# Performance work log

Measured on AMD Instinct MI355X. Metric: run time of the kernel, lower is better.

Reference implementation:

```python
import jax, jax.numpy as jnp
import numpy as np

B = 256
THRESH = 0.0
SHIFT = 0.0


def setup_inputs() -> dict:
    key = jax.random.key(0)
    ks = jax.random.split(key, 8)
    s = lambda k, shape, sc: (jax.random.normal(k, shape, jnp.float32) * sc)
    return {
        "x": jax.random.normal(ks[0], (B, 3, 250, 250), jnp.float32),
        "conv1_w": s(ks[1], (6, 3, 5, 5), 0.08),
        "conv1_b": jnp.zeros((6,), jnp.float32),
        "conv2_w": s(ks[2], (15, 6, 3, 3), 0.12),
        "conv2_b": jnp.zeros((15,), jnp.float32),
        "fc1_w": s(ks[3], (120, 55815), 0.004),
        "fc1_b": jnp.zeros((120,), jnp.float32),
        "fc2_w": s(ks[4], (84, 120), 0.09),
        "fc2_b": jnp.zeros((84,), jnp.float32),
        "fc3_w": s(ks[5], (1, 84), 0.1),
        "fc3_b": jnp.zeros((1,), jnp.float32),
        "pl_w": s(ks[6], (1, 1), 1.0),
        "pl_b": jnp.zeros((1,), jnp.float32),
        "pl_scale": jnp.ones((1,), jnp.float32),
        "pl_bias": jnp.zeros((1,), jnp.float32),
    }


def _conv2d(x, w, b, stride, pad):
    y = jax.lax.conv_general_dilated(
        x, w, (stride, stride), [(pad, pad), (pad, pad)],
        dimension_numbers=("NCHW", "OIHW", "NCHW"))
    return y + b[None, :, None, None]


def _maxpool_k2_s1(x):
    return jax.lax.reduce_window(x, -jnp.inf, jax.lax.max,
                                 (1, 1, 2, 2), (1, 1, 1, 1), "VALID")


def reference(x, conv1_w, conv1_b, conv2_w, conv2_b, fc1_w, fc1_b,
              fc2_w, fc2_b, fc3_w, fc3_b, pl_w, pl_b, pl_scale, pl_bias):
    # CNN backbone (dropout layers are eval-mode no-ops)
    h = jax.nn.relu(_conv2d(x, conv1_w, conv1_b, 2, 1))   # [B,6,124,124]
    h = _maxpool_k2_s1(h)                                  # [B,6,123,123]
    h = jax.nn.relu(_conv2d(h, conv2_w, conv2_b, 2, 1))   # [B,15,62,62]
    h = _maxpool_k2_s1(h)                                  # [B,15,61,61]
    h = h.reshape(h.shape[0], -1)                          # [B,55815]
    h = jax.nn.relu(h @ fc1_w.T + fc1_b)                   # [B,120]
    features = h @ fc2_w.T + fc2_b                         # [B,84]

    # head: fc3 -> ParameterizedLayer -> sigmoid
    logits = features @ fc3_w.T + fc3_b                    # [B,1]
    z = jnp.tanh(logits @ pl_w.T + pl_b) * pl_scale + pl_bias + SHIFT
    probs = jax.nn.sigmoid(z)[:, 0]                        # [B]

    # dynamic cosine-similarity graph (fidelity_adjacency, secondary=None)
    norms = jnp.linalg.norm(features, axis=1)              # [B]
    sim = (features @ features.T) / (norms[:, None] * norms[None, :] + 1e-12)
    adj = (sim >= THRESH) & (~jnp.eye(features.shape[0], dtype=bool))
    adjf = adj.astype(probs.dtype)                         # [B,B] 0/1

    # degree-weighted neighbor-mean aggregation
    deg = adjf.sum(axis=1)                                 # [B]
    neigh_mean = jnp.where(deg > 0, (adjf @ probs) / jnp.maximum(deg, 1.0), 0.0)
    agg = (probs + neigh_mean) / (1.0 + deg)
    return jnp.stack([agg, 1.0 - agg], axis=-1)            # [B,2]
```

## Files before the change

kernel.cpp:

```cpp
#include <hip/hip_runtime.h>
#include <math.h>


__global__ __launch_bounds__(256) void k_c1p1(const float* __restrict__ x,
                                              const float* __restrict__ w,
                                              const float* __restrict__ bias,
                                              float* __restrict__ p1) {
    __shared__ float xs[22][258];

    const int t    = blockIdx.x;
    const int b    = blockIdx.y;
    const int tid  = threadIdx.x;
    const int lane = tid & 63;
    const int wv   = tid >> 6;
    const int s    = wv & 1;
    const int q    = wv >> 1;
    const int ow   = 62 * s + lane;
    const int owc  = min(ow, 123);
    const int owc2 = 2 * owc;
    const int ihlo = 16 * t - 1;

    const int sr  = __builtin_amdgcn_readfirstlane(tid >> 7);
    const int sm  = tid & 127;
    const int smc = min(sm, 124);

    float acc[5][6];
#pragma unroll
    for (int j = 0; j < 5; ++j)
#pragma unroll
        for (int oc = 0; oc < 6; ++oc) acc[j][oc] = 0.f;

    const float* xb = x + (size_t)b * 3 * 62500;

#pragma unroll 1
    for (int ci = 0; ci < 3; ++ci) {
        __syncthreads();
        const float* xc = xb + (size_t)ci * 62500;
        float2 vv[11];
#pragma unroll
        for (int i = 0; i < 11; ++i) {
            int r   = 2 * i + sr;
            int ih  = ihlo + r;
            int ihc = min(max(ih, 0), 249);
            bool ok = (ih >= 0) && (ih < 250);
            float2 raw = *(const float2*)(xc + (size_t)ihc * 250 + (smc << 1));
            vv[i].x = ok ? raw.x : 0.f;
            vv[i].y = ok ? raw.y : 0.f;
        }
#pragma unroll
        for (int i = 0; i < 11; ++i) {
            int r = 2 * i + sr;
            xs[r][2 * sm + 1] = vv[i].x;
            xs[r][2 * sm + 2] = vv[i].y;
        }
        if (tid < 21) xs[tid][0] = 0.f;
        __syncthreads();

        float rr[7][5];
#pragma unroll
        for (int t7 = 0; t7 < 7; ++t7) {
            const float* pp = &xs[8 * q + 2 * t7][owc2];
            rr[t7][0] = pp[0]; rr[t7][1] = pp[1]; rr[t7][2] = pp[2];
            rr[t7][3] = pp[3]; rr[t7][4] = pp[4];
        }
#pragma unroll
        for (int kp = 0; kp < 3; ++kp) {
            const int kh = 2 * kp;
            float wk[6][5];
#pragma unroll
            for (int oc = 0; oc < 6; ++oc)
#pragma unroll
                for (int kw = 0; kw < 5; ++kw)
                    wk[oc][kw] = w[((oc * 3 + ci) * 5 + kh) * 5 + kw];
#pragma unroll
            for (int j = 0; j < 5; ++j) {
                const float* rp = rr[j + kp];
#pragma unroll
                for (int oc = 0; oc < 6; ++oc) {
                    float a = acc[j][oc];
                    a = fmaf(rp[0], wk[oc][0], a);
                    a = fmaf(rp[1], wk[oc][1], a);
                    a = fmaf(rp[2], wk[oc][2], a);
                    a = fmaf(rp[3], wk[oc][3], a);
                    a = fmaf(rp[4], wk[oc][4], a);
                    acc[j][oc] = a;
                }
            }
        }
#pragma unroll
        for (int t6 = 0; t6 < 6; ++t6) {
            const float* pp = &xs[8 * q + 2 * t6 + 1][owc2];
            rr[t6][0] = pp[0]; rr[t6][1] = pp[1]; rr[t6][2] = pp[2];
            rr[t6][3] = pp[3]; rr[t6][4] = pp[4];
        }
#pragma unroll
        for (int kp = 0; kp < 2; ++kp) {
            const int kh = 2 * kp + 1;
            float wk[6][5];
#pragma unroll
            for (int oc = 0; oc < 6; ++oc)
#pragma unroll
                for (int kw = 0; kw < 5; ++kw)
                    wk[oc][kw] = w[((oc * 3 + ci) * 5 + kh) * 5 + kw];
#pragma unroll
            for (int j = 0; j < 5; ++j) {
                const float* rp = rr[j + kp];
#pragma unroll
                for (int oc = 0; oc < 6; ++oc) {
                    float a = acc[j][oc];
                    a = fmaf(rp[0], wk[oc][0], a);
                    a = fmaf(rp[1], wk[oc][1], a);
                    a = fmaf(rp[2], wk[oc][2], a);
                    a = fmaf(rp[3], wk[oc][3], a);
                    a = fmaf(rp[4], wk[oc][4], a);
                    acc[j][oc] = a;
                }
            }
        }
    }

    const int pw   = ow;
    const int oh0  = 8 * t + 4 * q;
    const bool cok = (lane < 63) && (pw < 123);
#pragma unroll
    for (int oc = 0; oc < 6; ++oc) {
        float bv = bias[oc];
        float r0 = fmaxf(acc[0][oc] + bv, 0.f);
        float r1 = fmaxf(acc[1][oc] + bv, 0.f);
        float r2 = fmaxf(acc[2][oc] + bv, 0.f);
        float r3 = fmaxf(acc[3][oc] + bv, 0.f);
        float r4 = fmaxf(acc[4][oc] + bv, 0.f);
        float vm0 = fmaxf(r0, r1), vm1 = fmaxf(r1, r2);
        float vm2 = fmaxf(r2, r3), vm3 = fmaxf(r3, r4);
        float p0 = fmaxf(vm0, __shfl_down(vm0, 1));
        float p1v = fmaxf(vm1, __shfl_down(vm1, 1));
        float p2v = fmaxf(vm2, __shfl_down(vm2, 1));
        float p3 = fmaxf(vm3, __shfl_down(vm3, 1));
        if (cok) {
            float* op = p1 + (((size_t)b * 6 + oc) * 123) * 123 + pw;
            if (oh0 + 0 < 123) op[(size_t)(oh0 + 0) * 123] = p0;
            if (oh0 + 1 < 123) op[(size_t)(oh0 + 1) * 123] = p1v;
            if (oh0 + 2 < 123) op[(size_t)(oh0 + 2) * 123] = p2v;
            if (oh0 + 3 < 123) op[(size_t)(oh0 + 3) * 123] = p3;
        }
    }
}

__global__ __launch_bounds__(256) void k_c2p2(const float* __restrict__ p1,
                                              const float* __restrict__ w,
                                              const float* __restrict__ bias,
                                              float* __restrict__ p2) {
    __shared__ float xs[20][130];

    const int v    = blockIdx.x;
    const int b    = blockIdx.y;
    const int tid  = threadIdx.x;
    const int lane = tid & 63;
    const int q    = tid >> 6;
    const int ow   = lane;
    const int owc  = min(ow, 61);
    const int owc2 = 2 * owc;
    const int ihlo = 16 * v - 1;

    const int sr   = __builtin_amdgcn_readfirstlane(tid >> 7);
    const int sc   = tid & 127;
    const int scc  = min(sc, 122);
    const int wcol = (sc < 123) ? (sc + 1) : 129;

    float acc[3][15];
#pragma unroll
    for (int j = 0; j < 3; ++j)
#pragma unroll
        for (int oc = 0; oc < 15; ++oc) acc[j][oc] = 0.f;

    const float* ib = p1 + (size_t)b * 6 * 15129;

#pragma unroll 1
    for (int ci = 0; ci < 6; ++ci) {
        __syncthreads();
        const float* xc = ib + (size_t)ci * 15129;
        float vv[10];
#pragma unroll
        for (int i = 0; i < 10; ++i) {
            int r   = 2 * i + sr;
            int ih  = ihlo + r;
            int ihc = min(max(ih, 0), 122);
            bool ok = (ih >= 0) && (ih < 123);
            float raw = xc[(size_t)ihc * 123 + scc];
            vv[i] = ok ? raw : 0.f;
        }
#pragma unroll
        for (int i = 0; i < 10; ++i) {
            int r = 2 * i + sr;
            xs[r][wcol] = vv[i];
        }
        if (tid < 19) { xs[tid][0] = 0.f; xs[tid][124] = 0.f; }
        __syncthreads();

        float rr[7][3];
#pragma unroll
        for (int c = 0; c < 7; ++c) {
            const float* pp = &xs[4 * q + c][owc2];
            rr[c][0] = pp[0]; rr[c][1] = pp[1]; rr[c][2] = pp[2];
        }
#pragma unroll
        for (int kh = 0; kh < 3; ++kh) {
            float wk[15][3];
#pragma unroll
            for (int oc = 0; oc < 15; ++oc)
#pragma unroll
                for (int kw = 0; kw < 3; ++kw)
                    wk[oc][kw] = w[((oc * 6 + ci) * 3 + kh) * 3 + kw];
#pragma unroll
            for (int j = 0; j < 3; ++j) {
                const float* rp = rr[2 * j + kh];
#pragma unroll
                for (int oc = 0; oc < 15; ++oc) {
                    float a = acc[j][oc];
                    a = fmaf(rp[0], wk[oc][0], a);
                    a = fmaf(rp[1], wk[oc][1], a);
                    a = fmaf(rp[2], wk[oc][2], a);
                    acc[j][oc] = a;
                }
            }
        }
    }

    const int pw   = ow;
    const int oh0  = 8 * v + 2 * q;
    const bool cok = (lane < 61);
#pragma unroll
    for (int oc = 0; oc < 15; ++oc) {
        float bv = bias[oc];
        float r0 = fmaxf(acc[0][oc] + bv, 0.f);
        float r1 = fmaxf(acc[1][oc] + bv, 0.f);
        float r2 = fmaxf(acc[2][oc] + bv, 0.f);
        float vm0 = fmaxf(r0, r1), vm1 = fmaxf(r1, r2);
        float p0 = fmaxf(vm0, __shfl_down(vm0, 1));
        float p1v = fmaxf(vm1, __shfl_down(vm1, 1));
        if (cok) {
            float* op = p2 + (((size_t)b * 15 + oc) * 61) * 61 + pw;
            if (oh0 + 0 < 61) op[(size_t)(oh0 + 0) * 61] = p0;
            if (oh0 + 1 < 61) op[(size_t)(oh0 + 1) * 61] = p1v;
        }
    }
}

__global__ __launch_bounds__(256) void k_fc1(const float* __restrict__ A,
                                             const float* __restrict__ B,
                                             float* __restrict__ partial) {
    __shared__ float As[128][64];
    __shared__ float Bs[128][64];
    const int K = 55815;
    int tid = threadIdx.x;
    int kb  = blockIdx.x;
    int m0  = blockIdx.y * 128;
    int mx  = tid >> 4;
    int nx  = tid & 15;
    int kl  = tid & 63;
    int mb  = tid >> 6;

    Bs[120 + mb][kl] = 0.f;
    Bs[124 + mb][kl] = 0.f;

    float acc[8][8];
#pragma unroll
    for (int i = 0; i < 8; ++i)
#pragma unroll
        for (int j = 0; j < 8; ++j) acc[i][j] = 0.f;

    for (int ch = kb; ch < 873; ch += 256) {
        int k    = ch * 64 + kl;
        bool kok = (k < K);
        int kc   = kok ? k : K - 1;
        __syncthreads();
#pragma unroll
        for (int batch = 0; batch < 4; ++batch) {
            float va[8], vb[8];
#pragma unroll
            for (int u = 0; u < 8; ++u) {
                int m = mb + 4 * (batch * 8 + u);
                va[u] = A[(size_t)(m0 + m) * K + kc];
            }
#pragma unroll
            for (int u = 0; u < 8; ++u) {
                if (batch < 3 || u < 6) {
                    int m = mb + 4 * (batch * 8 + u);
                    vb[u] = B[(size_t)m * K + kc];
                }
            }
#pragma unroll
            for (int u = 0; u < 8; ++u) {
                int m = mb + 4 * (batch * 8 + u);
                As[m][kl ^ ((m & 7) << 2)] = kok ? va[u] : 0.f;
            }
#pragma unroll
            for (int u = 0; u < 8; ++u) {
                if (batch < 3 || u < 6) {
                    int m = mb + 4 * (batch * 8 + u);
                    Bs[m][kl ^ ((m & 7) << 2)] = kok ? vb[u] : 0.f;
                }
            }
        }
        __syncthreads();
#pragma unroll 2
        for (int k4 = 0; k4 < 16; ++k4) {
            float4 af[8], bf[8];
#pragma unroll
            for (int i = 0; i < 8; ++i) {
                int m = mx + 16 * i;
                af[i] = *(const float4*)&As[m][(k4 * 4) ^ ((m & 7) << 2)];
            }
#pragma unroll
            for (int j = 0; j < 8; ++j) {
                int n = nx + 16 * j;
                bf[j] = *(const float4*)&Bs[n][(k4 * 4) ^ ((n & 7) << 2)];
            }
#pragma unroll
            for (int i = 0; i < 8; ++i)
#pragma unroll
                for (int j = 0; j < 8; ++j) {
                    acc[i][j] = fmaf(af[i].x, bf[j].x, acc[i][j]);
                    acc[i][j] = fmaf(af[i].y, bf[j].y, acc[i][j]);
                    acc[i][j] = fmaf(af[i].z, bf[j].z, acc[i][j]);
                    acc[i][j] = fmaf(af[i].w, bf[j].w, acc[i][j]);
                }
        }
    }

    float* pp = partial + (size_t)kb * 30720;
#pragma unroll
    for (int i = 0; i < 8; ++i) {
        int m = m0 + mx + 16 * i;
#pragma unroll
        for (int j = 0; j < 8; ++j) {
            int n = nx + 16 * j;
            if (n < 120) pp[m * 120 + n] = acc[i][j];
        }
    }
}

__global__ __launch_bounds__(256) void k_fc1red(const float* __restrict__ partial,
                                                const float* __restrict__ bias,
                                                float* __restrict__ out) {
    int idx = blockIdx.x * 256 + threadIdx.x;
    int n = idx % 120;
    float s = bias[n];
#pragma unroll 8
    for (int kb = 0; kb < 256; ++kb) s += partial[(size_t)kb * 30720 + idx];
    out[idx] = fmaxf(s, 0.f);
}

__global__ __launch_bounds__(256) void k_fc2(const float* __restrict__ h,
                                             const float* __restrict__ w,
                                             const float* __restrict__ bias,
                                             float* __restrict__ out) {
    int idx = blockIdx.x * 256 + threadIdx.x;
    int n = idx % 84;
    int m = idx / 84;
    const float* hp = h + m * 120;
    const float* wp = w + n * 120;
    float s = bias[n];
#pragma unroll 4
    for (int k = 0; k < 120; ++k) s = fmaf(hp[k], wp[k], s);
    out[idx] = s;
}

__global__ __launch_bounds__(256) void k_head(const float* __restrict__ f,
                                              const float* __restrict__ w3,
                                              const float* __restrict__ b3,
                                              const float* __restrict__ plw,
                                              const float* __restrict__ plb,
                                              const float* __restrict__ pls,
                                              const float* __restrict__ plbias,
                                              float* __restrict__ probs,
                                              float* __restrict__ norms) {
    int b = threadIdx.x;
    const float* fp = f + b * 84;
    float nsq = 0.f, lg = b3[0];
#pragma unroll 4
    for (int k = 0; k < 84; ++k) {
        float v = fp[k];
        nsq = fmaf(v, v, nsq);
        lg  = fmaf(v, w3[k], lg);
    }
    float z = tanhf(lg * plw[0] + plb[0]) * pls[0] + plbias[0];
    probs[b] = 1.f / (1.f + expf(-z));
    norms[b] = sqrtf(nsq);
}

__global__ __launch_bounds__(256) void k_graph(const float* __restrict__ f,
                                               const float* __restrict__ probs,
                                               const float* __restrict__ norms,
                                               float* __restrict__ out) {
    __shared__ float fi[84];
    __shared__ float sd[4], sv[4];
    int i = blockIdx.x;
    int j = threadIdx.x;
    if (j < 84) fi[j] = f[i * 84 + j];
    __syncthreads();
    const float* fj = f + j * 84;
    float dot = 0.f;
#pragma unroll 4
    for (int k = 0; k < 84; ++k) dot = fmaf(fi[k], fj[k], dot);
    float sim = dot / (norms[i] * norms[j] + 1e-12f);
    bool adj = (j != i) && (sim >= 0.0f);
    float d = adj ? 1.f : 0.f;
    float v = adj ? probs[j] : 0.f;
#pragma unroll
    for (int off = 32; off >= 1; off >>= 1) {
        d += __shfl_down(d, off);
        v += __shfl_down(v, off);
    }
    int wave = j >> 6, lane = j & 63;
    if (lane == 0) { sd[wave] = d; sv[wave] = v; }
    __syncthreads();
    if (j == 0) {
        float D = sd[0] + sd[1] + sd[2] + sd[3];
        float V = sv[0] + sv[1] + sv[2] + sv[3];
        float nm = (D > 0.f) ? (V / fmaxf(D, 1.f)) : 0.f;
        float agg = (probs[i] + nm) / (1.f + D);
        out[2 * i]     = agg;
        out[2 * i + 1] = 1.f - agg;
    }
}

extern "C" void kernel_launch(void* const* d_in, const int* in_sizes, int n_in,
                              void* d_out, int out_size, void* d_ws, size_t ws_size,
                              hipStream_t stream) {
    const float* x    = (const float*)d_in[0];
    const float* w1   = (const float*)d_in[1];
    const float* b1   = (const float*)d_in[2];
    const float* w2   = (const float*)d_in[3];
    const float* b2   = (const float*)d_in[4];
    const float* fw1  = (const float*)d_in[5];
    const float* fb1  = (const float*)d_in[6];
    const float* fw2  = (const float*)d_in[7];
    const float* fb2  = (const float*)d_in[8];
    const float* fw3  = (const float*)d_in[9];
    const float* fb3  = (const float*)d_in[10];
    const float* plw  = (const float*)d_in[11];
    const float* plb  = (const float*)d_in[12];
    const float* pls  = (const float*)d_in[13];
    const float* plbi = (const float*)d_in[14];
    float* out = (float*)d_out;

    float* ws = (float*)d_ws;
    float* p1       = ws;
    float* p2       = p1 + 23238144;
    float* partial  = p2 + 14288640;
    float* fc1out   = partial + 7864320;
    float* features = fc1out + 30720;
    float* probs    = features + 21504;
    float* norms    = probs + 256;

    k_c1p1<<<dim3(16, 256), 256, 0, stream>>>(x, w1, b1, p1);
    k_c2p2<<<dim3(8, 256), 256, 0, stream>>>(p1, w2, b2, p2);
    k_fc1<<<dim3(256, 2), 256, 0, stream>>>(p2, fw1, partial);
    k_fc1red<<<120, 256, 0, stream>>>(partial, fb1, fc1out);
    k_fc2<<<84, 256, 0, stream>>>(fc1out, fw2, fb2, features);
    k_head<<<1, 256, 0, stream>>>(features, fw3, fb3, plw, plb, pls, plbi,
                                  probs, norms);
    k_graph<<<256, 256, 0, stream>>>(features, probs, norms, out);
}
```

Baseline: 488.3 us.

## Double-buffer conv and fc1 tiles with register prefetch, split fc1 reduction

Both conv kernels now use double-buffered shared memory tiles. The next input channel's rows are prefetched into registers while the current channel is computed, which removes one barrier per channel. The fc1 split-K GEMM now loads the next K-chunk into registers (va/vb arrays) before computing the current one, and launch bounds are added to cap register use. The single-pass fc1 partial reduction over 256 slices becomes a two-stage reduction spread across more blocks. The extra registers and the doubled shared memory may lower occupancy or cause spills.

```diff
diff --git a/kernel.cpp b/kernel.cpp
--- a/kernel.cpp
+++ b/kernel.cpp
@@ -2,11 +2,11 @@
 #include <math.h>
 
 
-__global__ __launch_bounds__(256) void k_c1p1(const float* __restrict__ x,
-                                              const float* __restrict__ w,
-                                              const float* __restrict__ bias,
-                                              float* __restrict__ p1) {
-    __shared__ float xs[22][258];
+__global__ __launch_bounds__(256, 3) void k_c1p1(const float* __restrict__ x,
+                                                 const float* __restrict__ w,
+                                                 const float* __restrict__ bias,
+                                                 float* __restrict__ p1) {
+    __shared__ float xs[2][22][258];
 
     const int t    = blockIdx.x;
     const int b    = blockIdx.y;
@@ -32,11 +32,9 @@
 
     const float* xb = x + (size_t)b * 3 * 62500;
 
-#pragma unroll 1
-    for (int ci = 0; ci < 3; ++ci) {
-        __syncthreads();
-        const float* xc = xb + (size_t)ci * 62500;
-        float2 vv[11];
+    float2 vv[11];
+    {
+        const float* xc = xb;
 #pragma unroll
         for (int i = 0; i < 11; ++i) {
             int r   = 2 * i + sr;
@@ -50,16 +48,35 @@
 #pragma unroll
         for (int i = 0; i < 11; ++i) {
             int r = 2 * i + sr;
-            xs[r][2 * sm + 1] = vv[i].x;
-            xs[r][2 * sm + 2] = vv[i].y;
-        }
-        if (tid < 21) xs[tid][0] = 0.f;
+            xs[0][r][2 * sm + 1] = vv[i].x;
+            xs[0][r][2 * sm + 2] = vv[i].y;
+        }
+        if (tid < 22) { xs[0][tid][0] = 0.f; xs[1][tid][0] = 0.f; }
+    }
+
+#pragma unroll
+    for (int ci = 0; ci < 3; ++ci) {
+        const int cur = ci & 1;
+        const int nxt = cur ^ 1;
+        if (ci < 2) {
+            const float* xc = xb + (size_t)(ci + 1) * 62500;
+#pragma unroll
+            for (int i = 0; i < 11; ++i) {
+                int r   = 2 * i + sr;
+                int ih  = ihlo + r;
+                int ihc = min(max(ih, 0), 249);
+                bool ok = (ih >= 0) && (ih < 250);
+                float2 raw = *(const float2*)(xc + (size_t)ihc * 250 + (smc << 1));
+                vv[i].x = ok ? raw.x : 0.f;
+                vv[i].y = ok ? raw.y : 0.f;
+            }
+        }
         __syncthreads();
 
         float rr[7][5];
 #pragma unroll
         for (int t7 = 0; t7 < 7; ++t7) {
-            const float* pp = &xs[8 * q + 2 * t7][owc2];
+            const float* pp = &xs[cur][8 * q + 2 * t7][owc2];
             rr[t7][0] = pp[0]; rr[t7][1] = pp[1]; rr[t7][2] = pp[2];
             rr[t7][3] = pp[3]; rr[t7][4] = pp[4];
         }
@@ -89,7 +106,7 @@
         }
 #pragma unroll
         for (int t6 = 0; t6 < 6; ++t6) {
-            const float* pp = &xs[8 * q + 2 * t6 + 1][owc2];
+            const float* pp = &xs[cur][8 * q + 2 * t6 + 1][owc2];
             rr[t6][0] = pp[0]; rr[t6][1] = pp[1]; rr[t6][2] = pp[2];
             rr[t6][3] = pp[3]; rr[t6][4] = pp[4];
         }
@@ -115,6 +132,15 @@
                     a = fmaf(rp[4], wk[oc][4], a);
                     acc[j][oc] = a;
                 }
+            }
+        }
+
+        if (ci < 2) {
+#pragma unroll
+            for (int i = 0; i < 11; ++i) {
+                int r = 2 * i + sr;
+                xs[nxt][r][2 * sm + 1] = vv[i].x;
+                xs[nxt][r][2 * sm + 2] = vv[i].y;
             }
         }
     }
@@ -146,11 +172,11 @@
     }
 }
 
-__global__ __launch_bounds__(256) void k_c2p2(const float* __restrict__ p1,
-                                              const float* __restrict__ w,
-                                              const float* __restrict__ bias,
-                                              float* __restrict__ p2) {
-    __shared__ float xs[20][130];
+__global__ __launch_bounds__(256, 3) void k_c2p2(const float* __restrict__ p1,
+                                                 const float* __restrict__ w,
+                                                 const float* __restrict__ bias,
+                                                 float* __restrict__ p2) {
+    __shared__ float xs[2][20][130];
 
     const int v    = blockIdx.x;
     const int b    = blockIdx.y;
@@ -175,11 +201,9 @@
 
     const float* ib = p1 + (size_t)b * 6 * 15129;
 
-#pragma unroll 1
-    for (int ci = 0; ci < 6; ++ci) {
-        __syncthreads();
-        const float* xc = ib + (size_t)ci * 15129;
-        float vv[10];
+    float vv[10];
+    {
+        const float* xc = ib;
 #pragma unroll
         for (int i = 0; i < 10; ++i) {
             int r   = 2 * i + sr;
@@ -192,15 +216,36 @@
 #pragma unroll
         for (int i = 0; i < 10; ++i) {
             int r = 2 * i + sr;
-            xs[r][wcol] = vv[i];
-        }
-        if (tid < 19) { xs[tid][0] = 0.f; xs[tid][124] = 0.f; }
+            xs[0][r][wcol] = vv[i];
+        }
+        if (tid < 20) {
+            xs[0][tid][0] = 0.f; xs[0][tid][124] = 0.f;
+            xs[1][tid][0] = 0.f; xs[1][tid][124] = 0.f;
+        }
+    }
+
+#pragma unroll
+    for (int ci = 0; ci < 6; ++ci) {
+        const int cur = ci & 1;
+        const int nxt = cur ^ 1;
+        if (ci < 5) {
+            const float* xc = ib + (size_t)(ci + 1) * 15129;
+#pragma unroll
+            for (int i = 0; i < 10; ++i) {
+                int r   = 2 * i + sr;
+                int ih  = ihlo + r;
+                int ihc = min(max(ih, 0), 122);
+                bool ok = (ih >= 0) && (ih < 123);
+                float raw = xc[(size_t)ihc * 123 + scc];
+                vv[i] = ok ? raw : 0.f;
+            }
+        }
         __syncthreads();
 
         float rr[7][3];
 #pragma unroll
         for (int c = 0; c < 7; ++c) {
-            const float* pp = &xs[4 * q + c][owc2];
+            const float* pp = &xs[cur][4 * q + c][owc2];
             rr[c][0] = pp[0]; rr[c][1] = pp[1]; rr[c][2] = pp[2];
         }
 #pragma unroll
@@ -222,6 +267,14 @@
                     a = fmaf(rp[2], wk[oc][2], a);
                     acc[j][oc] = a;
                 }
+            }
+        }
+
+        if (ci < 5) {
+#pragma unroll
+            for (int i = 0; i < 10; ++i) {
+                int r = 2 * i + sr;
+                xs[nxt][r][wcol] = vv[i];
             }
         }
     }
@@ -246,9 +299,9 @@
     }
 }
 
-__global__ __launch_bounds__(256) void k_fc1(const float* __restrict__ A,
-                                             const float* __restrict__ B,
-                                             float* __restrict__ partial) {
+__global__ __launch_bounds__(256, 2) void k_fc1(const float* __restrict__ A,
+                                                const float* __restrict__ B,
+                                                float* __restrict__ partial) {
     __shared__ float As[128][64];
     __shared__ float Bs[128][64];
     const int K = 55815;
@@ -269,38 +322,41 @@
 #pragma unroll
         for (int j = 0; j < 8; ++j) acc[i][j] = 0.f;
 
+    float va[32], vb[30];
+    {
+        int k    = kb * 64 + kl;
+        bool kok = (k < K);
+        int kc   = kok ? k : 0;
+#pragma unroll
+        for (int u = 0; u < 32; ++u)
+            va[u] = kok ? A[(size_t)(m0 + mb + 4 * u) * K + kc] : 0.f;
+#pragma unroll
+        for (int u = 0; u < 30; ++u)
+            vb[u] = kok ? B[(size_t)(mb + 4 * u) * K + kc] : 0.f;
+    }
+
     for (int ch = kb; ch < 873; ch += 256) {
-        int k    = ch * 64 + kl;
-        bool kok = (k < K);
-        int kc   = kok ? k : K - 1;
         __syncthreads();
 #pragma unroll
-        for (int batch = 0; batch < 4; ++batch) {
-            float va[8], vb[8];
-#pragma unroll
-            for (int u = 0; u < 8; ++u) {
-                int m = mb + 4 * (batch * 8 + u);
-                va[u] = A[(size_t)(m0 + m) * K + kc];
-            }
-#pragma unroll
-            for (int u = 0; u < 8; ++u) {
-                if (batch < 3 || u < 6) {
-                    int m = mb + 4 * (batch * 8 + u);
-                    vb[u] = B[(size_t)m * K + kc];
-                }
-            }
-#pragma unroll
-            for (int u = 0; u < 8; ++u) {
-                int m = mb + 4 * (batch * 8 + u);
-                As[m][kl ^ ((m & 7) << 2)] = kok ? va[u] : 0.f;
-            }
-#pragma unroll
-            for (int u = 0; u < 8; ++u) {
-                if (batch < 3 || u < 6) {
-                    int m = mb + 4 * (batch * 8 + u);
-                    Bs[m][kl ^ ((m & 7) << 2)] = kok ? vb[u] : 0.f;
-                }
-            }
+        for (int u = 0; u < 32; ++u) {
+            int m = mb + 4 * u;
+            As[m][kl ^ ((m & 7) << 2)] = va[u];
+        }
+#pragma unroll
+        for (int u = 0; u < 30; ++u) {
+            int m = mb + 4 * u;
+            Bs[m][kl ^ ((m & 7) << 2)] = vb[u];
+        }
+        if (ch + 256 < 873) {
+            int k    = (ch + 256) * 64 + kl;
+            bool kok = (k < K);
+            int kc   = kok ? k : 0;
+#pragma unroll
+            for (int u = 0; u < 32; ++u)
+                va[u] = kok ? A[(size_t)(m0 + mb + 4 * u) * K + kc] : 0.f;
+#pragma unroll
+            for (int u = 0; u < 30; ++u)
+                vb[u] = kok ? B[(size_t)(mb + 4 * u) * K + kc] : 0.f;
         }
         __syncthreads();
 #pragma unroll 2
@@ -340,14 +396,25 @@
     }
 }
 
-__global__ __launch_bounds__(256) void k_fc1red(const float* __restrict__ partial,
-                                                const float* __restrict__ bias,
-                                                float* __restrict__ out) {
+__global__ __launch_bounds__(256) void k_fc1red1(const float* __restrict__ partial,
+                                                 float* __restrict__ partial2) {
+    int idx = blockIdx.x * 256 + threadIdx.x;
+    int s   = blockIdx.y;
+    const float* p = partial + (size_t)(s * 32) * 30720 + idx;
+    float acc = 0.f;
+#pragma unroll 8
+    for (int kb = 0; kb < 32; ++kb) acc += p[(size_t)kb * 30720];
+    partial2[(size_t)s * 30720 + idx] = acc;
+}
+
+__global__ __launch_bounds__(256) void k_fc1red2(const float* __restrict__ partial2,
+                                                 const float* __restrict__ bias,
+                                                 float* __restrict__ out) {
     int idx = blockIdx.x * 256 + threadIdx.x;
     int n = idx % 120;
     float s = bias[n];
-#pragma unroll 8
-    for (int kb = 0; kb < 256; ++kb) s += partial[(size_t)kb * 30720 + idx];
+#pragma unroll
+    for (int k = 0; k < 8; ++k) s += partial2[(size_t)k * 30720 + idx];
     out[idx] = fmaxf(s, 0.f);
 }
 
@@ -453,11 +520,13 @@
     float* features = fc1out + 30720;
     float* probs    = features + 21504;
     float* norms    = probs + 256;
+    float* partial2 = norms + 256;
 
     k_c1p1<<<dim3(16, 256), 256, 0, stream>>>(x, w1, b1, p1);
     k_c2p2<<<dim3(8, 256), 256, 0, stream>>>(p1, w2, b2, p2);
     k_fc1<<<dim3(256, 2), 256, 0, stream>>>(p2, fw1, partial);
-    k_fc1red<<<120, 256, 0, stream>>>(partial, fb1, fc1out);
+    k_fc1red1<<<dim3(120, 8), 256, 0, stream>>>(partial, partial2);
+    k_fc1red2<<<120, 256, 0, stream>>>(partial2, fb1, fc1out);
     k_fc2<<<84, 256, 0, stream>>>(fc1out, fw2, fb2, features);
     k_head<<<1, 256, 0, stream>>>(features, fw3, fb3, plw, plb, pls, plbi,
                                   probs, norms);
```

Result: slower. 676.4 us (+38.5%).
